# Performance work log

Hardware: AMD Instinct MI355X
Metric: run time of the kernel (lower is better)

The kernel has to match this reference:

```python
import jax, jax.numpy as jnp
import numpy as np

N_EMB = 256
HEAD_SIZE = 64
B, S = 4, 4096


def setup_inputs() -> dict:
    key = jax.random.key(0)
    k1, k2, k3, k4 = jax.random.split(key, 4)
    return {
        "ini_emb": jax.random.normal(k1, (B, S, N_EMB), dtype=jnp.float32),
        "wk": jax.random.normal(k2, (N_EMB, HEAD_SIZE), dtype=jnp.float32) * (N_EMB ** -0.5),
        "wq": jax.random.normal(k3, (N_EMB, HEAD_SIZE), dtype=jnp.float32) * (N_EMB ** -0.5),
        "wv": jax.random.normal(k4, (N_EMB, HEAD_SIZE), dtype=jnp.float32) * (N_EMB ** -0.5),
    }


def reference(ini_emb, wk, wq, wv):
    # projections: [B,S,E] @ [E,H] -> [B,S,H]
    k = ini_emb @ wk
    q = ini_emb @ wq
    v = ini_emb @ wv
    # scores: [B,S,S]; NOTE: source scales by n_emb**-0.5, not head_size**-0.5
    scores = jnp.einsum("bqh,bkh->bqk", q, k) * (N_EMB ** -0.5)
    attn = jax.nn.softmax(scores, axis=-1)
    # output: [B,S,H]
    return jnp.einsum("bqk,bkh->bqh", attn, v)
```

## Files before the change

### kernel.cpp

```cpp
#include <hip/hip_runtime.h>


typedef short short4v __attribute__((ext_vector_type(4)));
typedef short short8v __attribute__((ext_vector_type(8)));
typedef float floatx4 __attribute__((ext_vector_type(4)));
typedef unsigned short u16;
typedef unsigned int u32;

#define SEQ 4096
#define EMB 256
#define HD 64
#define PADA 264
#define OSTR 68

static __device__ __forceinline__ u16 f2bf(float x) {
    union { float f; unsigned u; } v; v.f = x;
    unsigned r = v.u + 0x7FFFu + ((v.u >> 16) & 1u);
    return (u16)(r >> 16);
}

static __device__ __forceinline__ u32 cvt_pk_bf16(float a, float b) {
    u32 r;
    asm("v_cvt_pk_bf16_f32 %0, %1, %2" : "=v"(r) : "v"(a), "v"(b));
    return r;
}

static __device__ __forceinline__ short4v pack_bf4(float a, float b, float c, float d) {
    union { u32 u[2]; short4v s; } x;
    x.u[0] = cvt_pk_bf16(a, b);
    x.u[1] = cvt_pk_bf16(c, d);
    return x.s;
}

__global__ __launch_bounds__(256) void prep_w(
    const float* __restrict__ wk, const float* __restrict__ wq, const float* __restrict__ wv,
    u16* __restrict__ wt) {
    const int nt = blockIdx.x;
    const int t = threadIdx.x;
#pragma unroll
    for (int ss = 0; ss < 2; ++ss) {
        int slot = t + ss * 256;
        int kc = slot >> 6, lane = slot & 63;
        int ln15 = lane & 15, lq = lane >> 4;
        int cg = nt * 16 + ln15;
        int mat = cg >> 6, col = cg & 63;
        const float* W = (mat == 0) ? wq : (mat == 1) ? wk : wv;
        const float s = (mat == 0) ? 0.0625f * 1.44269504088896f : 1.0f;
        u32 w4[4];
#pragma unroll
        for (int p = 0; p < 2; ++p) {
#pragma unroll
            for (int d = 0; d < 2; ++d) {
                int e0 = kc * 32 + lq * 8 + p * 4 + d * 2;
                u16 lo = f2bf(W[(e0 + 0) * HD + col] * s);
                u16 hi = f2bf(W[(e0 + 1) * HD + col] * s);
                w4[p * 2 + d] = (u32)lo | ((u32)hi << 16);
            }
        }
        u32* dst = (u32*)wt + ((size_t)(nt * 8 + kc) * 64 + lane) * 4;
        *(uint4*)dst = make_uint4(w4[0], w4[1], w4[2], w4[3]);
    }
}

__global__ __launch_bounds__(256) void proj_mfma(
    const float* __restrict__ emb, const u16* __restrict__ wt,
    u16* __restrict__ qb, u16* __restrict__ kb, u16* __restrict__ vbt) {
    __shared__ u16 a_s[16 * PADA];
    const int t = threadIdx.x;
    const int lane = t & 63;
    const int wave = t >> 6;
    const int ln15 = lane & 15;
    const int lq = lane >> 4;
    const size_t row0 = (size_t)blockIdx.x * 16;

#pragma unroll
    for (int c = 0; c < 4; ++c) {
        int f = t + c * 256;
        int row = f >> 6, e4 = (f & 63) * 4;
        float4 v = *(const float4*)(emb + (row0 + row) * EMB + e4);
        u32 lo = cvt_pk_bf16(v.x, v.y);
        u32 hi = cvt_pk_bf16(v.z, v.w);
        *(uint2*)&a_s[row * PADA + e4] = make_uint2(lo, hi);
    }
    __syncthreads();

    floatx4 acc[3];
#pragma unroll
    for (int j = 0; j < 3; ++j) {
        floatx4 z = { 0.f, 0.f, 0.f, 0.f };
        acc[j] = z;
    }

#pragma unroll
    for (int kc = 0; kc < 8; ++kc) {
        short8v a = *(const short8v*)&a_s[ln15 * PADA + kc * 32 + lq * 8];
#pragma unroll
        for (int j = 0; j < 3; ++j) {
            short8v b = *(const short8v*)(wt + (((size_t)(wave * 3 + j) * 8 + kc) * 64 + lane) * 8);
            acc[j] = __builtin_amdgcn_mfma_f32_16x16x32_bf16(a, b, acc[j], 0, 0, 0);
        }
    }

#pragma unroll
    for (int j = 0; j < 3; ++j) {
        int cg = (wave * 3 + j) * 16 + ln15;
        int mat = cg >> 6, col = cg & 63;
        if (mat < 2) {
            u16* O = (mat == 0) ? qb : kb;
#pragma unroll
            for (int r = 0; r < 4; ++r)
                O[(row0 + lq * 4 + r) * HD + col] = f2bf(acc[j][r]);
        } else {
            u32 lo = cvt_pk_bf16(acc[j][0], acc[j][1]);
            u32 hi = cvt_pk_bf16(acc[j][2], acc[j][3]);
            size_t bidx = row0 >> 12;
            size_t sl = (row0 & 4095) + lq * 4;
            *(uint2*)&vbt[(bidx * 64 + col) * SEQ + sl] = make_uint2(lo, hi);
        }
    }
}


template <bool PF>
static __device__ __forceinline__ void attn_step(
    const int tt, const int split, const int wave, const int ln15, const int lq,
    const u16* __restrict__ kpb, const u16* __restrict__ vpb,
    const short8v (&qf)[4][2],
    const short8v k0c, const short8v k1c, const short4v (&vfc)[4],
    short8v& k0n, short8v& k1n, short4v (&vfn)[4],
    floatx4 (&oacc)[4][4], float (&lacc)[4]) {
    const int kw = (split * 32 + tt) * 64 + wave * 16;

    if (PF) {
        const int kwn = kw + 64;
#pragma unroll
        for (int ht = 0; ht < 4; ++ht)
            vfn[ht] = *(const short4v*)(vpb + (size_t)(ht * 16 + ln15) * SEQ + kwn + lq * 4);
        k0n = *(const short8v*)(kpb + (size_t)(kwn + ln15) * HD + lq * 8);
        k1n = *(const short8v*)(kpb + (size_t)(kwn + ln15) * HD + 32 + lq * 8);
    }

    floatx4 s[4];
    __builtin_amdgcn_s_setprio(1);
#pragma unroll
    for (int nt = 0; nt < 4; ++nt) {
        floatx4 z = { 0.f, 0.f, 0.f, 0.f };
        s[nt] = __builtin_amdgcn_mfma_f32_16x16x32_bf16(k0c, qf[nt][0], z, 0, 0, 0);
        s[nt] = __builtin_amdgcn_mfma_f32_16x16x32_bf16(k1c, qf[nt][1], s[nt], 0, 0, 0);
    }
    __builtin_amdgcn_s_setprio(0);

    short4v pf[4];
#pragma unroll
    for (int nt = 0; nt < 4; ++nt) {
        float p0 = __builtin_amdgcn_exp2f(s[nt][0]);
        float p1 = __builtin_amdgcn_exp2f(s[nt][1]);
        float p2 = __builtin_amdgcn_exp2f(s[nt][2]);
        float p3 = __builtin_amdgcn_exp2f(s[nt][3]);
        lacc[nt] += (p0 + p1) + (p2 + p3);
        pf[nt] = pack_bf4(p0, p1, p2, p3);
    }

    __builtin_amdgcn_s_setprio(1);
#pragma unroll
    for (int ht = 0; ht < 4; ++ht)
#pragma unroll
        for (int nt = 0; nt < 4; ++nt)
            oacc[ht][nt] = __builtin_amdgcn_mfma_f32_16x16x16bf16_1k(
                vfc[ht], pf[nt], oacc[ht][nt], 0, 0, 0);
    __builtin_amdgcn_s_setprio(0);
}

__global__ __launch_bounds__(256) void attn_kernel(
    const u16* __restrict__ qb, const u16* __restrict__ kb, const u16* __restrict__ vbt,
    float* __restrict__ po, float* __restrict__ pml) {
    __shared__ float ored[64 * OSTR];
    __shared__ float lred[4 * 64];

    const int t = threadIdx.x;
    const int lane = t & 63;
    const int wave = t >> 6;
    const int ln15 = lane & 15;
    const int lq = lane >> 4;

    const int part = ((blockIdx.x & 7) << 6) | (blockIdx.x >> 3);
    const int b = part >> 7;
    const int qt = (part >> 1) & 63;
    const int split = part & 1;
    const int q0 = qt * 64;

    const u16* __restrict__ qpb = qb + ((size_t)b * SEQ + q0) * HD;
    const u16* __restrict__ kpb = kb + (size_t)b * SEQ * HD;
    const u16* __restrict__ vpb = vbt + (size_t)b * HD * SEQ;

    short8v qf[4][2];
#pragma unroll
    for (int nt = 0; nt < 4; ++nt)
#pragma unroll
        for (int h = 0; h < 2; ++h)
            qf[nt][h] = *(const short8v*)(qpb + (size_t)(nt * 16 + ln15) * HD + h * 32 + lq * 8);

    floatx4 oacc[4][4];
#pragma unroll
    for (int ht = 0; ht < 4; ++ht)
#pragma unroll
        for (int nt = 0; nt < 4; ++nt) {
            floatx4 z = { 0.f, 0.f, 0.f, 0.f };
            oacc[ht][nt] = z;
        }
    float lacc[4] = { 0.f, 0.f, 0.f, 0.f };

    short8v kA0, kA1, kB0, kB1;
    short4v vfA[4], vfB[4];
    {
        const int kw0 = (split * 32) * 64 + wave * 16;
        kA0 = *(const short8v*)(kpb + (size_t)(kw0 + ln15) * HD + lq * 8);
        kA1 = *(const short8v*)(kpb + (size_t)(kw0 + ln15) * HD + 32 + lq * 8);
#pragma unroll
        for (int ht = 0; ht < 4; ++ht)
            vfA[ht] = *(const short4v*)(vpb + (size_t)(ht * 16 + ln15) * SEQ + kw0 + lq * 4);
    }

#pragma unroll 1
    for (int tth = 0; tth < 15; ++tth) {
        attn_step<true>(2 * tth,     split, wave, ln15, lq, kpb, vpb, qf,
                        kA0, kA1, vfA, kB0, kB1, vfB, oacc, lacc);
        attn_step<true>(2 * tth + 1, split, wave, ln15, lq, kpb, vpb, qf,
                        kB0, kB1, vfB, kA0, kA1, vfA, oacc, lacc);
    }
    attn_step<true >(30, split, wave, ln15, lq, kpb, vpb, qf,
                     kA0, kA1, vfA, kB0, kB1, vfB, oacc, lacc);
    attn_step<false>(31, split, wave, ln15, lq, kpb, vpb, qf,
                     kB0, kB1, vfB, kA0, kA1, vfA, oacc, lacc);

#pragma unroll
    for (int nt = 0; nt < 4; ++nt) {
        lacc[nt] += __shfl_xor(lacc[nt], 16);
        lacc[nt] += __shfl_xor(lacc[nt], 32);
    }
    if (lq == 0) {
#pragma unroll
        for (int nt = 0; nt < 4; ++nt)
            lred[wave * 64 + nt * 16 + ln15] = lacc[nt];
    }

    for (int s4 = 0; s4 < 4; ++s4) {
        if (wave == s4) {
#pragma unroll
            for (int nt = 0; nt < 4; ++nt)
#pragma unroll
                for (int ht = 0; ht < 4; ++ht) {
                    int idx = (nt * 16 + ln15) * OSTR + ht * 16 + lq * 4;
                    if (s4 == 0) {
                        *(floatx4*)&ored[idx] = oacc[ht][nt];
                    } else {
                        floatx4 old = *(floatx4*)&ored[idx];
                        old += oacc[ht][nt];
                        *(floatx4*)&ored[idx] = old;
                    }
                }
        }
        __syncthreads();
    }

    float* __restrict__ pob = po + (size_t)part * 4096;
#pragma unroll
    for (int i = 0; i < 4; ++i) {
        int f4 = t + i * 256;
        int q = f4 >> 4, h4 = (f4 & 15) * 4;
        *(float4*)&pob[q * HD + h4] = *(float4*)&ored[q * OSTR + h4];
    }
    if (t < 64)
        pml[part * 64 + t] = lred[t] + lred[64 + t] + lred[128 + t] + lred[192 + t];
}

__global__ __launch_bounds__(256) void reduce_kernel(
    const float* __restrict__ po, const float* __restrict__ pml,
    float* __restrict__ out) {
    __shared__ float ls[64];
    const int t = threadIdx.x;
    const int part0 = blockIdx.x * 2;
    const int bq = blockIdx.x;

    if (t < 64)
        ls[t] = pml[(part0 + 0) * 64 + t] + pml[(part0 + 1) * 64 + t];
    __syncthreads();

    const float* __restrict__ p0 = po + (size_t)(part0 + 0) * 4096;
    const float* __restrict__ p1 = po + (size_t)(part0 + 1) * 4096;
    float* __restrict__ ob = out + (((size_t)(bq >> 6) * SEQ + (size_t)(bq & 63) * 64)) * HD;

#pragma unroll
    for (int i = 0; i < 4; ++i) {
        int f4 = t + i * 256;
        int f = f4 * 4;
        int q = f4 >> 4;
        float4 a = *(const float4*)&p0[f];
        float4 c = *(const float4*)&p1[f];
        float inv = 1.0f / ls[q];
        float4 r;
        r.x = (a.x + c.x) * inv;
        r.y = (a.y + c.y) * inv;
        r.z = (a.z + c.z) * inv;
        r.w = (a.w + c.w) * inv;
        *(float4*)&ob[f] = r;
    }
}

extern "C" void kernel_launch(void* const* d_in, const int* in_sizes, int n_in,
                              void* d_out, int out_size, void* d_ws, size_t ws_size,
                              hipStream_t stream) {
    const float* emb = (const float*)d_in[0];
    const float* wk  = (const float*)d_in[1];
    const float* wq  = (const float*)d_in[2];
    const float* wv  = (const float*)d_in[3];

    u16* qb  = (u16*)d_ws;
    u16* kb  = (u16*)((char*)d_ws + (size_t)2 * 1024 * 1024);
    u16* vbt = (u16*)((char*)d_ws + (size_t)4 * 1024 * 1024);
    u16* wt  = (u16*)((char*)d_ws + (size_t)6 * 1024 * 1024);
    float* po  = (float*)((char*)d_ws + (size_t)6 * 1024 * 1024 + 256 * 1024);
    float* pml = (float*)((char*)d_ws + (size_t)22 * 1024 * 1024 + 256 * 1024);
    float* out = (float*)d_out;

    prep_w<<<12, 256, 0, stream>>>(wk, wq, wv, wt);
    proj_mfma<<<1024, 256, 0, stream>>>(emb, wt, qb, kb, vbt);
    attn_kernel<<<512, 256, 0, stream>>>(qb, kb, vbt, po, pml);
    reduce_kernel<<<256, 256, 0, stream>>>(po, pml, out);
}
```

Before: 131.4 us.

## Switch attention inner loop to 32x32x16 MFMA with permlane32 P repacking

Replaces the 16x16 MFMA tiling in the attention step with 32x32x16 bf16 MFMAs. Each wave now owns a 32-query by 32-key tile: waves split into key halves and query halves. The scores to P conversion uses v_permlane32_swap to put the accumulator layout into B-operand layout without going through LDS. The cross-wave reduction shrinks from four serialized passes to two. The aim is fewer MFMA issues with higher per-instruction throughput and less reduction overhead, at the cost of larger per-wave register tiles and extra permlane instructions.

```diff
diff --git a/kernel.cpp b/kernel.cpp
--- a/kernel.cpp
+++ b/kernel.cpp
@@ -4,6 +4,7 @@
 typedef short short4v __attribute__((ext_vector_type(4)));
 typedef short short8v __attribute__((ext_vector_type(8)));
 typedef float floatx4 __attribute__((ext_vector_type(4)));
+typedef float floatx16 __attribute__((ext_vector_type(16)));
 typedef unsigned short u16;
 typedef unsigned int u32;
 
@@ -23,13 +24,6 @@
     u32 r;
     asm("v_cvt_pk_bf16_f32 %0, %1, %2" : "=v"(r) : "v"(a), "v"(b));
     return r;
-}
-
-static __device__ __forceinline__ short4v pack_bf4(float a, float b, float c, float d) {
-    union { u32 u[2]; short4v s; } x;
-    x.u[0] = cvt_pk_bf16(a, b);
-    x.u[1] = cvt_pk_bf16(c, d);
-    return x.s;
 }
 
 __global__ __launch_bounds__(256) void prep_w(
@@ -123,65 +117,72 @@
 
 template <bool PF>
 static __device__ __forceinline__ void attn_step(
-    const int tt, const int split, const int wave, const int ln15, const int lq,
+    const int tt, const int split, const int kh, const int ln31, const int hi8,
     const u16* __restrict__ kpb, const u16* __restrict__ vpb,
-    const short8v (&qf)[4][2],
-    const short8v k0c, const short8v k1c, const short4v (&vfc)[4],
-    short8v& k0n, short8v& k1n, short4v (&vfn)[4],
-    floatx4 (&oacc)[4][4], float (&lacc)[4]) {
-    const int kw = (split * 32 + tt) * 64 + wave * 16;
+    const short8v (&qf)[4],
+    const short8v (&kfc)[4], const short8v (&vfc)[2][2],
+    short8v (&kfn)[4], short8v (&vfn)[2][2],
+    floatx16 (&oacc)[2], float& lacc) {
+    const int kw = (split * 32 + tt) * 64 + kh * 32;
 
     if (PF) {
         const int kwn = kw + 64;
 #pragma unroll
-        for (int ht = 0; ht < 4; ++ht)
-            vfn[ht] = *(const short4v*)(vpb + (size_t)(ht * 16 + ln15) * SEQ + kwn + lq * 4);
-        k0n = *(const short8v*)(kpb + (size_t)(kwn + ln15) * HD + lq * 8);
-        k1n = *(const short8v*)(kpb + (size_t)(kwn + ln15) * HD + 32 + lq * 8);
-    }
-
-    floatx4 s[4];
+        for (int ch = 0; ch < 4; ++ch)
+            kfn[ch] = *(const short8v*)(kpb + (size_t)(kwn + ln31) * HD + ch * 16 + hi8);
+#pragma unroll
+        for (int ht = 0; ht < 2; ++ht)
+#pragma unroll
+            for (int ks = 0; ks < 2; ++ks)
+                vfn[ht][ks] = *(const short8v*)(vpb + (size_t)(ht * 32 + ln31) * SEQ + kwn + ks * 16 + hi8);
+    }
+
+    floatx16 c = { 0.f, 0.f, 0.f, 0.f, 0.f, 0.f, 0.f, 0.f,
+                   0.f, 0.f, 0.f, 0.f, 0.f, 0.f, 0.f, 0.f };
     __builtin_amdgcn_s_setprio(1);
 #pragma unroll
-    for (int nt = 0; nt < 4; ++nt) {
-        floatx4 z = { 0.f, 0.f, 0.f, 0.f };
-        s[nt] = __builtin_amdgcn_mfma_f32_16x16x32_bf16(k0c, qf[nt][0], z, 0, 0, 0);
-        s[nt] = __builtin_amdgcn_mfma_f32_16x16x32_bf16(k1c, qf[nt][1], s[nt], 0, 0, 0);
-    }
+    for (int ch = 0; ch < 4; ++ch)
+        c = __builtin_amdgcn_mfma_f32_32x32x16_bf16(kfc[ch], qf[ch], c, 0, 0, 0);
     __builtin_amdgcn_s_setprio(0);
 
-    short4v pf[4];
-#pragma unroll
-    for (int nt = 0; nt < 4; ++nt) {
-        float p0 = __builtin_amdgcn_exp2f(s[nt][0]);
-        float p1 = __builtin_amdgcn_exp2f(s[nt][1]);
-        float p2 = __builtin_amdgcn_exp2f(s[nt][2]);
-        float p3 = __builtin_amdgcn_exp2f(s[nt][3]);
-        lacc[nt] += (p0 + p1) + (p2 + p3);
-        pf[nt] = pack_bf4(p0, p1, p2, p3);
-    }
-
-    __builtin_amdgcn_s_setprio(1);
-#pragma unroll
-    for (int ht = 0; ht < 4; ++ht)
-#pragma unroll
-        for (int nt = 0; nt < 4; ++nt)
-            oacc[ht][nt] = __builtin_amdgcn_mfma_f32_16x16x16bf16_1k(
-                vfc[ht], pf[nt], oacc[ht][nt], 0, 0, 0);
-    __builtin_amdgcn_s_setprio(0);
+    float p[16];
+#pragma unroll
+    for (int r = 0; r < 16; ++r)
+        p[r] = __builtin_amdgcn_exp2f(c[r]);
+    lacc += ((((p[0] + p[1]) + (p[2] + p[3])) + ((p[4] + p[5]) + (p[6] + p[7])))
+          + (((p[8] + p[9]) + (p[10] + p[11])) + ((p[12] + p[13]) + (p[14] + p[15]))));
+
+#pragma unroll
+    for (int ks = 0; ks < 2; ++ks) {
+        u32 a0 = cvt_pk_bf16(p[ks * 8 + 0], p[ks * 8 + 1]);
+        u32 a1 = cvt_pk_bf16(p[ks * 8 + 2], p[ks * 8 + 3]);
+        u32 a2 = cvt_pk_bf16(p[ks * 8 + 4], p[ks * 8 + 5]);
+        u32 a3 = cvt_pk_bf16(p[ks * 8 + 6], p[ks * 8 + 7]);
+        asm("v_permlane32_swap_b32 %0, %1" : "+v"(a0), "+v"(a2));
+        asm("v_permlane32_swap_b32 %0, %1" : "+v"(a1), "+v"(a3));
+        union { u32 w[4]; short8v s; } pb;
+        pb.w[0] = a0; pb.w[1] = a1; pb.w[2] = a2; pb.w[3] = a3;
+        __builtin_amdgcn_s_setprio(1);
+#pragma unroll
+        for (int ht = 0; ht < 2; ++ht)
+            oacc[ht] = __builtin_amdgcn_mfma_f32_32x32x16_bf16(vfc[ht][ks], pb.s, oacc[ht], 0, 0, 0);
+        __builtin_amdgcn_s_setprio(0);
+    }
 }
 
 __global__ __launch_bounds__(256) void attn_kernel(
     const u16* __restrict__ qb, const u16* __restrict__ kb, const u16* __restrict__ vbt,
     float* __restrict__ po, float* __restrict__ pml) {
     __shared__ float ored[64 * OSTR];
-    __shared__ float lred[4 * 64];
+    __shared__ float lred[128];
 
     const int t = threadIdx.x;
     const int lane = t & 63;
     const int wave = t >> 6;
-    const int ln15 = lane & 15;
-    const int lq = lane >> 4;
+    const int ln31 = lane & 31;
+    const int hi8 = (lane >> 5) * 8;
+    const int kh = wave >> 1;
+    const int qh = wave & 1;
 
     const int part = ((blockIdx.x & 7) << 6) | (blockIdx.x >> 3);
     const int b = part >> 7;
@@ -189,79 +190,80 @@
     const int split = part & 1;
     const int q0 = qt * 64;
 
-    const u16* __restrict__ qpb = qb + ((size_t)b * SEQ + q0) * HD;
+    const u16* __restrict__ qpb = qb + ((size_t)b * SEQ + q0 + qh * 32) * HD;
     const u16* __restrict__ kpb = kb + (size_t)b * SEQ * HD;
     const u16* __restrict__ vpb = vbt + (size_t)b * HD * SEQ;
 
-    short8v qf[4][2];
-#pragma unroll
-    for (int nt = 0; nt < 4; ++nt)
-#pragma unroll
-        for (int h = 0; h < 2; ++h)
-            qf[nt][h] = *(const short8v*)(qpb + (size_t)(nt * 16 + ln15) * HD + h * 32 + lq * 8);
-
-    floatx4 oacc[4][4];
-#pragma unroll
-    for (int ht = 0; ht < 4; ++ht)
-#pragma unroll
-        for (int nt = 0; nt < 4; ++nt) {
-            floatx4 z = { 0.f, 0.f, 0.f, 0.f };
-            oacc[ht][nt] = z;
-        }
-    float lacc[4] = { 0.f, 0.f, 0.f, 0.f };
-
-    short8v kA0, kA1, kB0, kB1;
-    short4v vfA[4], vfB[4];
+    short8v qf[4];
+#pragma unroll
+    for (int ch = 0; ch < 4; ++ch)
+        qf[ch] = *(const short8v*)(qpb + (size_t)ln31 * HD + ch * 16 + hi8);
+
+    floatx16 oacc[2];
+#pragma unroll
+    for (int ht = 0; ht < 2; ++ht) {
+        floatx16 z = { 0.f, 0.f, 0.f, 0.f, 0.f, 0.f, 0.f, 0.f,
+                       0.f, 0.f, 0.f, 0.f, 0.f, 0.f, 0.f, 0.f };
+        oacc[ht] = z;
+    }
+    float lacc = 0.f;
+
+    short8v kfA[4], kfB[4], vfA[2][2], vfB[2][2];
     {
-        const int kw0 = (split * 32) * 64 + wave * 16;
-        kA0 = *(const short8v*)(kpb + (size_t)(kw0 + ln15) * HD + lq * 8);
-        kA1 = *(const short8v*)(kpb + (size_t)(kw0 + ln15) * HD + 32 + lq * 8);
-#pragma unroll
-        for (int ht = 0; ht < 4; ++ht)
-            vfA[ht] = *(const short4v*)(vpb + (size_t)(ht * 16 + ln15) * SEQ + kw0 + lq * 4);
+        const int kw0 = (split * 32) * 64 + kh * 32;
+#pragma unroll
+        for (int ch = 0; ch < 4; ++ch)
+            kfA[ch] = *(const short8v*)(kpb + (size_t)(kw0 + ln31) * HD + ch * 16 + hi8);
+#pragma unroll
+        for (int ht = 0; ht < 2; ++ht)
+#pragma unroll
+            for (int ks = 0; ks < 2; ++ks)
+                vfA[ht][ks] = *(const short8v*)(vpb + (size_t)(ht * 32 + ln31) * SEQ + kw0 + ks * 16 + hi8);
     }
 
 #pragma unroll 1
     for (int tth = 0; tth < 15; ++tth) {
-        attn_step<true>(2 * tth,     split, wave, ln15, lq, kpb, vpb, qf,
-                        kA0, kA1, vfA, kB0, kB1, vfB, oacc, lacc);
-        attn_step<true>(2 * tth + 1, split, wave, ln15, lq, kpb, vpb, qf,
-                        kB0, kB1, vfB, kA0, kA1, vfA, oacc, lacc);
-    }
-    attn_step<true >(30, split, wave, ln15, lq, kpb, vpb, qf,
-                     kA0, kA1, vfA, kB0, kB1, vfB, oacc, lacc);
-    attn_step<false>(31, split, wave, ln15, lq, kpb, vpb, qf,
-                     kB0, kB1, vfB, kA0, kA1, vfA, oacc, lacc);
-
-#pragma unroll
-    for (int nt = 0; nt < 4; ++nt) {
-        lacc[nt] += __shfl_xor(lacc[nt], 16);
-        lacc[nt] += __shfl_xor(lacc[nt], 32);
-    }
-    if (lq == 0) {
-#pragma unroll
-        for (int nt = 0; nt < 4; ++nt)
-            lred[wave * 64 + nt * 16 + ln15] = lacc[nt];
-    }
-
-    for (int s4 = 0; s4 < 4; ++s4) {
-        if (wave == s4) {
-#pragma unroll
-            for (int nt = 0; nt < 4; ++nt)
-#pragma unroll
-                for (int ht = 0; ht < 4; ++ht) {
-                    int idx = (nt * 16 + ln15) * OSTR + ht * 16 + lq * 4;
-                    if (s4 == 0) {
-                        *(floatx4*)&ored[idx] = oacc[ht][nt];
-                    } else {
-                        floatx4 old = *(floatx4*)&ored[idx];
-                        old += oacc[ht][nt];
-                        *(floatx4*)&ored[idx] = old;
-                    }
-                }
-        }
-        __syncthreads();
-    }
+        attn_step<true>(2 * tth,     split, kh, ln31, hi8, kpb, vpb, qf,
+                        kfA, vfA, kfB, vfB, oacc, lacc);
+        attn_step<true>(2 * tth + 1, split, kh, ln31, hi8, kpb, vpb, qf,
+                        kfB, vfB, kfA, vfA, oacc, lacc);
+    }
+    attn_step<true >(30, split, kh, ln31, hi8, kpb, vpb, qf,
+                     kfA, vfA, kfB, vfB, oacc, lacc);
+    attn_step<false>(31, split, kh, ln31, hi8, kpb, vpb, qf,
+                     kfB, vfB, kfA, vfA, oacc, lacc);
+
+    lacc += __shfl_xor(lacc, 32);
+    if (lane < 32) lred[wave * 32 + ln31] = lacc;
+
+    if (kh == 0) {
+#pragma unroll
+        for (int ht = 0; ht < 2; ++ht)
+#pragma unroll
+            for (int g = 0; g < 4; ++g) {
+                int h = ht * 32 + g * 8 + (hi8 >> 1);
+                int idx = (qh * 32 + ln31) * OSTR + h;
+                floatx4 v4 = { oacc[ht][g * 4 + 0], oacc[ht][g * 4 + 1],
+                               oacc[ht][g * 4 + 2], oacc[ht][g * 4 + 3] };
+                *(floatx4*)&ored[idx] = v4;
+            }
+    }
+    __syncthreads();
+    if (kh == 1) {
+#pragma unroll
+        for (int ht = 0; ht < 2; ++ht)
+#pragma unroll
+            for (int g = 0; g < 4; ++g) {
+                int h = ht * 32 + g * 8 + (hi8 >> 1);
+                int idx = (qh * 32 + ln31) * OSTR + h;
+                floatx4 old = *(floatx4*)&ored[idx];
+                floatx4 v4 = { oacc[ht][g * 4 + 0], oacc[ht][g * 4 + 1],
+                               oacc[ht][g * 4 + 2], oacc[ht][g * 4 + 3] };
+                old += v4;
+                *(floatx4*)&ored[idx] = old;
+            }
+    }
+    __syncthreads();
 
     float* __restrict__ pob = po + (size_t)part * 4096;
 #pragma unroll
@@ -271,7 +273,7 @@
         *(float4*)&pob[q * HD + h4] = *(float4*)&ored[q * OSTR + h4];
     }
     if (t < 64)
-        pml[part * 64 + t] = lred[t] + lred[64 + t] + lred[128 + t] + lred[192 + t];
+        pml[part * 64 + t] = lred[t] + lred[64 + t];
 }
 
 __global__ __launch_bounds__(256) void reduce_kernel(
```

Measured after the change: 141.4 us. 7.6% more time.

## Stage K/V tiles through swizzled double-buffered LDS with coalesced loads

Applied to the files above, without the earlier changes.

Replaces the per-wave direct-to-register K/V fragment loads with cooperative 16-byte global loads of each 64-key K and V tile. The tiles are written into XOR-swizzled, double-buffered shared memory, and the MFMA fragments are then read from LDS. The output-reduction buffer now aliases the same shared memory. The aim is to replace narrow, strided V loads with coalesced ones. The cost is an LDS round trip and a block-wide barrier every iteration, even though each wave still consumes distinct keys, so there is no cross-wave reuse.

```diff
diff --git a/kernel.cpp b/kernel.cpp
--- a/kernel.cpp
+++ b/kernel.cpp
@@ -121,60 +121,10 @@
 }
 
 
-template <bool PF>
-static __device__ __forceinline__ void attn_step(
-    const int tt, const int split, const int wave, const int ln15, const int lq,
-    const u16* __restrict__ kpb, const u16* __restrict__ vpb,
-    const short8v (&qf)[4][2],
-    const short8v k0c, const short8v k1c, const short4v (&vfc)[4],
-    short8v& k0n, short8v& k1n, short4v (&vfn)[4],
-    floatx4 (&oacc)[4][4], float (&lacc)[4]) {
-    const int kw = (split * 32 + tt) * 64 + wave * 16;
-
-    if (PF) {
-        const int kwn = kw + 64;
-#pragma unroll
-        for (int ht = 0; ht < 4; ++ht)
-            vfn[ht] = *(const short4v*)(vpb + (size_t)(ht * 16 + ln15) * SEQ + kwn + lq * 4);
-        k0n = *(const short8v*)(kpb + (size_t)(kwn + ln15) * HD + lq * 8);
-        k1n = *(const short8v*)(kpb + (size_t)(kwn + ln15) * HD + 32 + lq * 8);
-    }
-
-    floatx4 s[4];
-    __builtin_amdgcn_s_setprio(1);
-#pragma unroll
-    for (int nt = 0; nt < 4; ++nt) {
-        floatx4 z = { 0.f, 0.f, 0.f, 0.f };
-        s[nt] = __builtin_amdgcn_mfma_f32_16x16x32_bf16(k0c, qf[nt][0], z, 0, 0, 0);
-        s[nt] = __builtin_amdgcn_mfma_f32_16x16x32_bf16(k1c, qf[nt][1], s[nt], 0, 0, 0);
-    }
-    __builtin_amdgcn_s_setprio(0);
-
-    short4v pf[4];
-#pragma unroll
-    for (int nt = 0; nt < 4; ++nt) {
-        float p0 = __builtin_amdgcn_exp2f(s[nt][0]);
-        float p1 = __builtin_amdgcn_exp2f(s[nt][1]);
-        float p2 = __builtin_amdgcn_exp2f(s[nt][2]);
-        float p3 = __builtin_amdgcn_exp2f(s[nt][3]);
-        lacc[nt] += (p0 + p1) + (p2 + p3);
-        pf[nt] = pack_bf4(p0, p1, p2, p3);
-    }
-
-    __builtin_amdgcn_s_setprio(1);
-#pragma unroll
-    for (int ht = 0; ht < 4; ++ht)
-#pragma unroll
-        for (int nt = 0; nt < 4; ++nt)
-            oacc[ht][nt] = __builtin_amdgcn_mfma_f32_16x16x16bf16_1k(
-                vfc[ht], pf[nt], oacc[ht][nt], 0, 0, 0);
-    __builtin_amdgcn_s_setprio(0);
-}
-
 __global__ __launch_bounds__(256) void attn_kernel(
     const u16* __restrict__ qb, const u16* __restrict__ kb, const u16* __restrict__ vbt,
     float* __restrict__ po, float* __restrict__ pml) {
-    __shared__ float ored[64 * OSTR];
+    __shared__ __align__(16) u16 smem[4][64 * 64];
     __shared__ float lred[4 * 64];
 
     const int t = threadIdx.x;
@@ -210,28 +160,93 @@
         }
     float lacc[4] = { 0.f, 0.f, 0.f, 0.f };
 
-    short8v kA0, kA1, kB0, kB1;
-    short4v vfA[4], vfB[4];
+    const int r0 = t >> 3, c0 = t & 7;
+    const int r1 = (t + 256) >> 3, c1 = t & 7;
+    const int sw0 = r0 * 64 + ((c0 ^ (r0 & 7)) * 8);
+    const int sw1 = r1 * 64 + ((c1 ^ (r1 & 7)) * 8);
+
+    const int krow = wave * 16 + ln15;
+    const int ksw_lo = krow * 64 + (((0 + lq) ^ (ln15 & 7)) * 8);
+    const int ksw_hi = krow * 64 + (((4 + lq) ^ (ln15 & 7)) * 8);
+    const int vch = wave * 2 + (lq >> 1);
+    const int voff = ((vch ^ (ln15 & 7)) * 8) + (lq & 1) * 4;
+
+    uint4 ka, kb4, va, vb4;
     {
-        const int kw0 = (split * 32) * 64 + wave * 16;
-        kA0 = *(const short8v*)(kpb + (size_t)(kw0 + ln15) * HD + lq * 8);
-        kA1 = *(const short8v*)(kpb + (size_t)(kw0 + ln15) * HD + 32 + lq * 8);
+        const int kwb = (split * 32) * 64;
+        ka  = *(const uint4*)(kpb + (size_t)(kwb + r0) * HD + c0 * 8);
+        kb4 = *(const uint4*)(kpb + (size_t)(kwb + r1) * HD + c1 * 8);
+        va  = *(const uint4*)(vpb + (size_t)r0 * SEQ + kwb + c0 * 8);
+        vb4 = *(const uint4*)(vpb + (size_t)r1 * SEQ + kwb + c1 * 8);
+        *(uint4*)(&smem[0][0] + sw0) = ka;
+        *(uint4*)(&smem[0][0] + sw1) = kb4;
+        *(uint4*)(&smem[1][0] + sw0) = va;
+        *(uint4*)(&smem[1][0] + sw1) = vb4;
+    }
+    __syncthreads();
+
+#pragma unroll 1
+    for (int tt = 0; tt < 32; ++tt) {
+        const int buf = tt & 1;
+        if (tt < 31) {
+            const int kwb = (split * 32 + tt + 1) * 64;
+            ka  = *(const uint4*)(kpb + (size_t)(kwb + r0) * HD + c0 * 8);
+            kb4 = *(const uint4*)(kpb + (size_t)(kwb + r1) * HD + c1 * 8);
+            va  = *(const uint4*)(vpb + (size_t)r0 * SEQ + kwb + c0 * 8);
+            vb4 = *(const uint4*)(vpb + (size_t)r1 * SEQ + kwb + c1 * 8);
+        }
+
+        const u16* kt = &smem[buf * 2 + 0][0];
+        const u16* vt = &smem[buf * 2 + 1][0];
+
+        short4v vf[4];
 #pragma unroll
         for (int ht = 0; ht < 4; ++ht)
-            vfA[ht] = *(const short4v*)(vpb + (size_t)(ht * 16 + ln15) * SEQ + kw0 + lq * 4);
-    }
-
-#pragma unroll 1
-    for (int tth = 0; tth < 15; ++tth) {
-        attn_step<true>(2 * tth,     split, wave, ln15, lq, kpb, vpb, qf,
-                        kA0, kA1, vfA, kB0, kB1, vfB, oacc, lacc);
-        attn_step<true>(2 * tth + 1, split, wave, ln15, lq, kpb, vpb, qf,
-                        kB0, kB1, vfB, kA0, kA1, vfA, oacc, lacc);
-    }
-    attn_step<true >(30, split, wave, ln15, lq, kpb, vpb, qf,
-                     kA0, kA1, vfA, kB0, kB1, vfB, oacc, lacc);
-    attn_step<false>(31, split, wave, ln15, lq, kpb, vpb, qf,
-                     kB0, kB1, vfB, kA0, kA1, vfA, oacc, lacc);
+            vf[ht] = *(const short4v*)(vt + (ht * 16 + ln15) * 64 + voff);
+
+        short8v k0 = *(const short8v*)(kt + ksw_lo);
+        short8v k1 = *(const short8v*)(kt + ksw_hi);
+
+        floatx4 s[4];
+        __builtin_amdgcn_s_setprio(1);
+#pragma unroll
+        for (int nt = 0; nt < 4; ++nt) {
+            floatx4 z = { 0.f, 0.f, 0.f, 0.f };
+            s[nt] = __builtin_amdgcn_mfma_f32_16x16x32_bf16(k0, qf[nt][0], z, 0, 0, 0);
+            s[nt] = __builtin_amdgcn_mfma_f32_16x16x32_bf16(k1, qf[nt][1], s[nt], 0, 0, 0);
+        }
+        __builtin_amdgcn_s_setprio(0);
+
+        short4v pf[4];
+#pragma unroll
+        for (int nt = 0; nt < 4; ++nt) {
+            float p0 = __builtin_amdgcn_exp2f(s[nt][0]);
+            float p1 = __builtin_amdgcn_exp2f(s[nt][1]);
+            float p2 = __builtin_amdgcn_exp2f(s[nt][2]);
+            float p3 = __builtin_amdgcn_exp2f(s[nt][3]);
+            lacc[nt] += (p0 + p1) + (p2 + p3);
+            pf[nt] = pack_bf4(p0, p1, p2, p3);
+        }
+
+        __builtin_amdgcn_s_setprio(1);
+#pragma unroll
+        for (int ht = 0; ht < 4; ++ht)
+#pragma unroll
+            for (int nt = 0; nt < 4; ++nt)
+                oacc[ht][nt] = __builtin_amdgcn_mfma_f32_16x16x16bf16_1k(
+                    vf[ht], pf[nt], oacc[ht][nt], 0, 0, 0);
+        __builtin_amdgcn_s_setprio(0);
+
+        if (tt < 31) {
+            u16* ktn = &smem[(buf ^ 1) * 2 + 0][0];
+            u16* vtn = &smem[(buf ^ 1) * 2 + 1][0];
+            *(uint4*)(ktn + sw0) = ka;
+            *(uint4*)(ktn + sw1) = kb4;
+            *(uint4*)(vtn + sw0) = va;
+            *(uint4*)(vtn + sw1) = vb4;
+        }
+        __syncthreads();
+    }
 
 #pragma unroll
     for (int nt = 0; nt < 4; ++nt) {
@@ -244,6 +259,7 @@
             lred[wave * 64 + nt * 16 + ln15] = lacc[nt];
     }
 
+    float* ored = (float*)&smem[0][0];
     for (int s4 = 0; s4 < 4; ++s4) {
         if (wave == s4) {
 #pragma unroll
```

New measurement: 112.7 us. 1.17x faster.
